# Kernel tuning notes

Hardware: AMD Instinct MI355X
Metric: run time of the kernel (lower is better)

Reference implementation:

```python
import jax, jax.numpy as jnp
import numpy as np

NV, NC = 100000, 50000        # num variables, num constraints
DV, DC = 8, 16                # padded neighbor-list widths
DIN, DH = 32, 128             # init_input_dim, output_dim (=init_output_dim)
NUM_LAYERS = 3                # aggregate loop runs num_layers-1 times
DCAT = 2 * DH + DIN           # input_dim of fc_variable/fc_constraint


def setup_inputs() -> dict:
    key = jax.random.key(0)
    ks = jax.random.split(key, 10)
    w = lambda k, shape: (jax.random.normal(k, shape, jnp.float32) * 0.05)
    return {
        "x": jax.random.normal(ks[0], (NV + NC, DIN), jnp.float32),
        "var_constr_index": jax.random.randint(ks[1], (NV, DV), 0, NC, dtype=jnp.int32),
        "constr_var_index": jax.random.randint(ks[2], (NC, DC), 0, NV, dtype=jnp.int32),
        "W_init_v": w(ks[3], (DIN, DH)), "b_init_v": jnp.zeros((DH,), jnp.float32),
        "W_init_c": w(ks[4], (DIN, DH)), "b_init_c": jnp.zeros((DH,), jnp.float32),
        "W_var": w(ks[5], (DCAT, DH)), "b_var": jnp.zeros((DH,), jnp.float32),
        "W_con": w(ks[6], (DCAT, DH)), "b_con": jnp.zeros((DH,), jnp.float32),
        "W_q": w(ks[7], (2 * DH, 1)), "b_q": jnp.zeros((1,), jnp.float32),
    }


def reference(x, var_constr_index, constr_var_index,
              W_init_v, b_init_v, W_init_c, b_init_c,
              W_var, b_var, W_con, b_con, W_q, b_q):
    nv = var_constr_index.shape[0]
    xv, xc = x[:nv], x[nv:]
    # layer zero init (fc_init_variables / fc_init_constraints)
    v = xv @ W_init_v + b_init_v          # [NV, DH]
    c = xc @ W_init_c + b_init_c          # [NC, DH]
    # message-passing layers: both updates read OLD v and OLD c
    for _ in range(1, NUM_LAYERS):
        agg_c = jnp.sum(v[constr_var_index], axis=1)   # [NC, DH] gather+sum over variable neighbors
        agg_v = jnp.sum(c[var_constr_index], axis=1)   # [NV, DH] gather+sum over constraint neighbors
        c_new = jnp.concatenate([agg_c, c, xc], axis=1) @ W_con + b_con
        v_new = jnp.concatenate([agg_v, v, xv], axis=1) @ W_var + b_var
        c, v = c_new, v_new
    # embedding_Q: global sum of variable features, broadcast, concat, linear
    g = jnp.sum(v, axis=0)                             # [DH]
    q_in = jnp.concatenate([jnp.broadcast_to(g, v.shape), v], axis=1)  # [NV, 2*DH]
    return q_in @ W_q + b_q                            # [NV, 1]
```

## Files before the change

kernel.cpp:

```cpp
#include <hip/hip_runtime.h>

#define NV 100000
#define NC 50000
#define DVAR 8
#define DCON 16

using short8 = __attribute__((ext_vector_type(8))) short;
using f32x4  = __attribute__((ext_vector_type(4))) float;

typedef const __attribute__((address_space(1))) void* as1cv;
typedef __attribute__((address_space(3))) void* as3v;

__device__ __forceinline__ unsigned short f2bf(float f) {
    union { float f; unsigned int u; } v; v.f = f;
    return (unsigned short)((v.u + 0x7fffu + ((v.u >> 16) & 1u)) >> 16);
}
__device__ __forceinline__ float bflo(unsigned int u) {
    union { unsigned int u; float f; } v; v.u = u << 16; return v.f;
}
__device__ __forceinline__ float bfhi(unsigned int u) {
    union { unsigned int u; float f; } v; v.u = u & 0xffff0000u; return v.f;
}

__global__ __launch_bounds__(256) void pack_kernel(
    const float* __restrict__ Wvar, const float* __restrict__ Wcon,
    const float* __restrict__ Wiv,  const float* __restrict__ Wic,
    unsigned short* __restrict__ WbVar, unsigned short* __restrict__ WbCon,
    unsigned short* __restrict__ WbIv,  unsigned short* __restrict__ WbIc,
    float* __restrict__ S)
{
    const int tid = blockIdx.x * 256 + threadIdx.x;
    for (int i = tid; i < 9 * 128 * 32; i += gridDim.x * 256) {
        int s = i >> 12, rem = i & 4095, c = rem >> 5, k = rem & 31;
        int src = (s * 32 + k) * 128 + c;
        WbVar[i] = f2bf(Wvar[src]);
        WbCon[i] = f2bf(Wcon[src]);
    }
    for (int i = tid; i < 128 * 32; i += gridDim.x * 256) {
        int c = i >> 5, k = i & 31;
        int src = k * 128 + c;
        WbIv[i] = f2bf(Wiv[src]);
        WbIc[i] = f2bf(Wic[src]);
    }
    if (tid == 0) S[0] = 0.f;
}

__global__ __launch_bounds__(256) void init_mfma(
    const float* __restrict__ x,
    const unsigned short* __restrict__ Wb,
    const float* __restrict__ bias,
    unsigned short* __restrict__ hout, int M)
{
    const int t = threadIdx.x;
    const int lane = t & 63;
    const int w = t >> 6;
    const int lrow = lane & 15;
    const int lg = lane >> 4;
    const int wrow0 = blockIdx.x * 64 + w * 16;
    int arow = wrow0 + lrow;
    int arowc = arow < M ? arow : M - 1;

    const float4* xp = (const float4*)(x + (size_t)arowc * 32 + lg * 8);
    float4 xa = xp[0], xb = xp[1];
    short8 afr;
    afr[0] = (short)f2bf(xa.x); afr[1] = (short)f2bf(xa.y);
    afr[2] = (short)f2bf(xa.z); afr[3] = (short)f2bf(xa.w);
    afr[4] = (short)f2bf(xb.x); afr[5] = (short)f2bf(xb.y);
    afr[6] = (short)f2bf(xb.z); afr[7] = (short)f2bf(xb.w);

    #pragma unroll
    for (int ct = 0; ct < 8; ++ct) {
        int c = ct * 16 + lrow;
        short8 bfr = *(const short8*)(Wb + (size_t)c * 32 + lg * 8);
        f32x4 acc = {0.f, 0.f, 0.f, 0.f};
        acc = __builtin_amdgcn_mfma_f32_16x16x32_bf16(afr, bfr, acc, 0, 0, 0);
        float bv = bias[c];
        #pragma unroll
        for (int r = 0; r < 4; ++r) {
            int orow = wrow0 + lg * 4 + r;
            if (orow < M) hout[(size_t)orow * 128 + c] = f2bf(acc[r] + bv);
        }
    }
}

template<int DEG>
__global__ __launch_bounds__(256) void agg_bf16(
    const unsigned short* __restrict__ hnb, const int* __restrict__ idx,
    unsigned short* __restrict__ agg, int M)
{
    const int tid = blockIdx.x * 256 + threadIdx.x;
    const int row = tid >> 4;
    const int part = tid & 15;
    if (row >= M) return;
    int nb[DEG];
    #pragma unroll
    for (int d4 = 0; d4 < DEG / 4; ++d4)
        *(int4*)(&nb[d4 * 4]) = *(const int4*)(idx + (size_t)row * DEG + d4 * 4);
    float a0=0.f,a1=0.f,a2=0.f,a3=0.f,a4=0.f,a5=0.f,a6=0.f,a7=0.f;
    #pragma unroll
    for (int b = 0; b < DEG; b += 8) {
        uint4 q[8];
        #pragma unroll
        for (int j = 0; j < 8; ++j)
            q[j] = *(const uint4*)(hnb + (size_t)nb[b + j] * 128 + part * 8);
        #pragma unroll
        for (int j = 0; j < 8; ++j) {
            a0 += bflo(q[j].x); a1 += bfhi(q[j].x);
            a2 += bflo(q[j].y); a3 += bfhi(q[j].y);
            a4 += bflo(q[j].z); a5 += bfhi(q[j].z);
            a6 += bflo(q[j].w); a7 += bfhi(q[j].w);
        }
    }
    uint4 o;
    o.x = (unsigned)f2bf(a0) | ((unsigned)f2bf(a1) << 16);
    o.y = (unsigned)f2bf(a2) | ((unsigned)f2bf(a3) << 16);
    o.z = (unsigned)f2bf(a4) | ((unsigned)f2bf(a5) << 16);
    o.w = (unsigned)f2bf(a6) | ((unsigned)f2bf(a7) << 16);
    *(uint4*)(agg + (size_t)row * 128 + part * 8) = o;
}

template<bool FINAL>
__global__ __launch_bounds__(256, 2) void gemm_mfma(
    const unsigned short* hself,
    const unsigned short* __restrict__ aggin,
    const float* __restrict__ xself,
    const unsigned short* __restrict__ Wb,
    const float* __restrict__ bias,
    unsigned short* hout,
    const float* __restrict__ Wq, float* __restrict__ S, float* __restrict__ dotout,
    int M)
{
    __shared__ __align__(16) unsigned short Aagg[64 * 128];
    __shared__ __align__(16) unsigned short Aself[64 * 128];
    __shared__ float red[4];
    const int t = threadIdx.x;
    const int lane = t & 63;
    const int w = t >> 6;
    const int lrow = lane & 15;
    const int lg = lane >> 4;
    const int r0 = blockIdx.x * 64;
    const int wrow0 = r0 + w * 16;
    const int arow = wrow0 + lrow;
    const int arowc = arow < M ? arow : M - 1;

    short8 xfr;
    {
        const float4* xp = (const float4*)(xself + (size_t)arowc * 32 + lg * 8);
        float4 xa = xp[0], xb = xp[1];
        xfr[0] = (short)f2bf(xa.x); xfr[1] = (short)f2bf(xa.y);
        xfr[2] = (short)f2bf(xa.z); xfr[3] = (short)f2bf(xa.w);
        xfr[4] = (short)f2bf(xb.x); xfr[5] = (short)f2bf(xb.y);
        xfr[6] = (short)f2bf(xb.z); xfr[7] = (short)f2bf(xb.w);
    }

    #pragma unroll
    for (int i = 0; i < 4; ++i) {
        int L = i * 256 + t;
        int row = L >> 4, c = L & 15;
        int gr = r0 + row;
        int grc = gr < M ? gr : M - 1;
        int cs = c ^ (row & 7);
        __builtin_amdgcn_global_load_lds(
            (as1cv)(aggin + (size_t)grc * 128 + cs * 8),
            (as3v)(&Aagg[(size_t)L * 8]), 16, 0, 0);
        __builtin_amdgcn_global_load_lds(
            (as1cv)(hself + (size_t)grc * 128 + cs * 8),
            (as3v)(&Aself[(size_t)L * 8]), 16, 0, 0);
    }

    short8 bfr[2][8];
    #pragma unroll
    for (int ct = 0; ct < 8; ++ct)
        bfr[0][ct] = *(const short8*)(Wb + (size_t)(ct * 16 + lrow) * 32 + lg * 8);

    __syncthreads();

    auto ldsA = [&](const unsigned short* base, int srel) -> short8 {
        int chunk = (4 * srel + lg) ^ (lrow & 7);
        return *(const short8*)(base + ((size_t)(w * 16 + lrow) * 16 + chunk) * 8);
    };

    f32x4 acc[8];
    #pragma unroll
    for (int ct = 0; ct < 8; ++ct) acc[ct] = (f32x4){0.f, 0.f, 0.f, 0.f};

    short8 afr = ldsA(Aagg, 0);
    #pragma unroll
    for (int s = 0; s < 9; ++s) {
        const int cur = s & 1, nxt = cur ^ 1;
        short8 afr_nxt;
        if (s < 8) {
            #pragma unroll
            for (int ct = 0; ct < 8; ++ct)
                bfr[nxt][ct] = *(const short8*)(
                    Wb + ((size_t)(s + 1) * 128 + ct * 16 + lrow) * 32 + lg * 8);
            afr_nxt = (s + 1 < 4) ? ldsA(Aagg, s + 1)
                    : (s + 1 < 8) ? ldsA(Aself, s + 1 - 4)
                                  : xfr;
        }
        #pragma unroll
        for (int ct = 0; ct < 8; ++ct)
            acc[ct] = __builtin_amdgcn_mfma_f32_16x16x32_bf16(afr, bfr[cur][ct], acc[ct], 0, 0, 0);
        afr = afr_nxt;
    }

    if (!FINAL) {
        #pragma unroll
        for (int ct = 0; ct < 8; ++ct) {
            int c = ct * 16 + lrow;
            float bv = bias[c];
            #pragma unroll
            for (int r = 0; r < 4; ++r) {
                int orow = wrow0 + lg * 4 + r;
                if (orow < M) hout[(size_t)orow * 128 + c] = f2bf(acc[ct][r] + bv);
            }
        }
    } else {
        float d0[4] = {0.f, 0.f, 0.f, 0.f};
        float d1[4] = {0.f, 0.f, 0.f, 0.f};
        #pragma unroll
        for (int ct = 0; ct < 8; ++ct) {
            int c = ct * 16 + lrow;
            float bv = bias[c];
            float wq0 = Wq[c];
            float wq1 = Wq[128 + c];
            #pragma unroll
            for (int r = 0; r < 4; ++r) {
                int orow = wrow0 + lg * 4 + r;
                float val = (orow < M) ? (acc[ct][r] + bv) : 0.f;
                d0[r] += val * wq0;
                d1[r] += val * wq1;
            }
        }
        #pragma unroll
        for (int r = 0; r < 4; ++r) {
            d0[r] += __shfl_xor(d0[r], 1); d0[r] += __shfl_xor(d0[r], 2);
            d0[r] += __shfl_xor(d0[r], 4); d0[r] += __shfl_xor(d0[r], 8);
            d1[r] += __shfl_xor(d1[r], 1); d1[r] += __shfl_xor(d1[r], 2);
            d1[r] += __shfl_xor(d1[r], 4); d1[r] += __shfl_xor(d1[r], 8);
        }
        if (lrow == 0) {
            #pragma unroll
            for (int r = 0; r < 4; ++r) {
                int orow = wrow0 + lg * 4 + r;
                if (orow < M) dotout[orow] = d1[r];
            }
        }
        float tot = d0[0] + d0[1] + d0[2] + d0[3];
        tot += __shfl_xor(tot, 16);
        tot += __shfl_xor(tot, 32);
        if (lane == 0) red[w] = tot;
        __syncthreads();
        if (t == 0) atomicAdd(S, red[0] + red[1] + red[2] + red[3]);
    }
}

__global__ __launch_bounds__(256) void addout_kernel(
    float* __restrict__ outp, const float* __restrict__ S,
    const float* __restrict__ bq, int n)
{
    int i = blockIdx.x * 256 + threadIdx.x;
    if (i < n) outp[i] = outp[i] + S[0] + bq[0];
}

extern "C" void kernel_launch(void* const* d_in, const int* in_sizes, int n_in,
                              void* d_out, int out_size, void* d_ws, size_t ws_size,
                              hipStream_t stream)
{
    const float* x    = (const float*)d_in[0];
    const int*   vci  = (const int*)  d_in[1];
    const int*   cvi  = (const int*)  d_in[2];
    const float* Wiv  = (const float*)d_in[3];
    const float* biv  = (const float*)d_in[4];
    const float* Wic  = (const float*)d_in[5];
    const float* bic  = (const float*)d_in[6];
    const float* Wvar = (const float*)d_in[7];
    const float* bvar = (const float*)d_in[8];
    const float* Wcon = (const float*)d_in[9];
    const float* bcon = (const float*)d_in[10];
    const float* Wq   = (const float*)d_in[11];
    const float* bq   = (const float*)d_in[12];
    float* outp = (float*)d_out;

    unsigned short* us = (unsigned short*)d_ws;
    size_t o = 0;
    unsigned short* vA    = us + o; o += (size_t)NV * 128;
    unsigned short* cA    = us + o; o += (size_t)NC * 128;
    unsigned short* cB    = us + o; o += (size_t)NC * 128;
    unsigned short* aggV  = us + o; o += (size_t)NV * 128;
    unsigned short* aggC  = us + o; o += (size_t)NC * 128;
    unsigned short* WbVar = us + o; o += 9 * 128 * 32;
    unsigned short* WbCon = us + o; o += 9 * 128 * 32;
    unsigned short* WbIv  = us + o; o += 128 * 32;
    unsigned short* WbIc  = us + o; o += 128 * 32;
    float* S = (float*)(us + o);

    const float* xc = x + (size_t)NV * 32;

    pack_kernel<<<144, 256, 0, stream>>>(Wvar, Wcon, Wiv, Wic, WbVar, WbCon, WbIv, WbIc, S);
    init_mfma<<<(NV + 63) / 64, 256, 0, stream>>>(x,  WbIv, biv, vA, NV);
    init_mfma<<<(NC + 63) / 64, 256, 0, stream>>>(xc, WbIc, bic, cA, NC);

    agg_bf16<DCON><<<(NC * 16 + 255) / 256, 256, 0, stream>>>(vA, cvi, aggC, NC);
    agg_bf16<DVAR><<<(NV * 16 + 255) / 256, 256, 0, stream>>>(cA, vci, aggV, NV);
    gemm_mfma<false><<<(NC + 63) / 64, 256, 0, stream>>>(
        cA, aggC, xc, WbCon, bcon, cB, nullptr, nullptr, nullptr, NC);
    gemm_mfma<false><<<(NV + 63) / 64, 256, 0, stream>>>(
        vA, aggV, x, WbVar, bvar, vA, nullptr, nullptr, nullptr, NV);

    agg_bf16<DVAR><<<(NV * 16 + 255) / 256, 256, 0, stream>>>(cB, vci, aggV, NV);
    gemm_mfma<true><<<(NV + 63) / 64, 256, 0, stream>>>(
        vA, aggV, x, WbVar, bvar, nullptr, Wq, S, outp, NV);

    addout_kernel<<<(NV + 255) / 256, 256, 0, stream>>>(outp, S, bq, NV);
}
```

Baseline: 298.3 us.

## Make GEMM persistent with double-buffered LDS tiles and pre-packed bf16 x

The fused GEMM kernel becomes persistent on a fixed 512-block grid. Each block loops over row tiles and stages the next tile's aggregate, self features and x into a second LDS buffer while computing the current one. A new kernel converts x to bf16 once up front, so the GEMMs load it straight into LDS and no longer convert floats per block. The aim is to hide global-load latency behind MFMA work and remove the repeated conversion, at the cost of an extra launch and roughly twice the LDS per block, which may limit occupancy.

```diff
diff --git a/kernel.cpp b/kernel.cpp
--- a/kernel.cpp
+++ b/kernel.cpp
@@ -43,6 +43,21 @@
         WbIc[i] = f2bf(Wic[src]);
     }
     if (tid == 0) S[0] = 0.f;
+}
+
+__global__ __launch_bounds__(256) void xpack_kernel(
+    const float* __restrict__ x, unsigned short* __restrict__ xb, int n8)
+{
+    int i = blockIdx.x * 256 + threadIdx.x;
+    if (i >= n8) return;
+    const float4* p = (const float4*)(x + (size_t)i * 8);
+    float4 a = p[0], b = p[1];
+    uint4 o;
+    o.x = (unsigned)f2bf(a.x) | ((unsigned)f2bf(a.y) << 16);
+    o.y = (unsigned)f2bf(a.z) | ((unsigned)f2bf(a.w) << 16);
+    o.z = (unsigned)f2bf(b.x) | ((unsigned)f2bf(b.y) << 16);
+    o.w = (unsigned)f2bf(b.z) | ((unsigned)f2bf(b.w) << 16);
+    *(uint4*)(xb + (size_t)i * 8) = o;
 }
 
 __global__ __launch_bounds__(256) void init_mfma(
@@ -123,133 +138,159 @@
 __global__ __launch_bounds__(256, 2) void gemm_mfma(
     const unsigned short* hself,
     const unsigned short* __restrict__ aggin,
-    const float* __restrict__ xself,
+    const unsigned short* __restrict__ xbself,
     const unsigned short* __restrict__ Wb,
     const float* __restrict__ bias,
     unsigned short* hout,
     const float* __restrict__ Wq, float* __restrict__ S, float* __restrict__ dotout,
     int M)
 {
-    __shared__ __align__(16) unsigned short Aagg[64 * 128];
-    __shared__ __align__(16) unsigned short Aself[64 * 128];
+    __shared__ __align__(16) unsigned short A0a[64 * 128], A0s[64 * 128];
+    __shared__ __align__(16) unsigned short A1a[64 * 128], A1s[64 * 128];
+    __shared__ __align__(16) unsigned short X0[64 * 32],  X1[64 * 32];
     __shared__ float red[4];
     const int t = threadIdx.x;
     const int lane = t & 63;
     const int w = t >> 6;
     const int lrow = lane & 15;
     const int lg = lane >> 4;
-    const int r0 = blockIdx.x * 64;
-    const int wrow0 = r0 + w * 16;
-    const int arow = wrow0 + lrow;
-    const int arowc = arow < M ? arow : M - 1;
-
-    short8 xfr;
-    {
-        const float4* xp = (const float4*)(xself + (size_t)arowc * 32 + lg * 8);
-        float4 xa = xp[0], xb = xp[1];
-        xfr[0] = (short)f2bf(xa.x); xfr[1] = (short)f2bf(xa.y);
-        xfr[2] = (short)f2bf(xa.z); xfr[3] = (short)f2bf(xa.w);
-        xfr[4] = (short)f2bf(xb.x); xfr[5] = (short)f2bf(xb.y);
-        xfr[6] = (short)f2bf(xb.z); xfr[7] = (short)f2bf(xb.w);
-    }
-
-    #pragma unroll
-    for (int i = 0; i < 4; ++i) {
-        int L = i * 256 + t;
-        int row = L >> 4, c = L & 15;
-        int gr = r0 + row;
-        int grc = gr < M ? gr : M - 1;
-        int cs = c ^ (row & 7);
-        __builtin_amdgcn_global_load_lds(
-            (as1cv)(aggin + (size_t)grc * 128 + cs * 8),
-            (as3v)(&Aagg[(size_t)L * 8]), 16, 0, 0);
-        __builtin_amdgcn_global_load_lds(
-            (as1cv)(hself + (size_t)grc * 128 + cs * 8),
-            (as3v)(&Aself[(size_t)L * 8]), 16, 0, 0);
-    }
-
-    short8 bfr[2][8];
-    #pragma unroll
-    for (int ct = 0; ct < 8; ++ct)
-        bfr[0][ct] = *(const short8*)(Wb + (size_t)(ct * 16 + lrow) * 32 + lg * 8);
-
-    __syncthreads();
-
-    auto ldsA = [&](const unsigned short* base, int srel) -> short8 {
-        int chunk = (4 * srel + lg) ^ (lrow & 7);
-        return *(const short8*)(base + ((size_t)(w * 16 + lrow) * 16 + chunk) * 8);
+    const int ntiles = (M + 63) >> 6;
+
+    float Sacc = 0.f;
+
+    auto stage = [&](unsigned short* La, unsigned short* Ls, unsigned short* Lx, int tile) {
+        const int r0 = tile * 64;
+        #pragma unroll
+        for (int i = 0; i < 4; ++i) {
+            int L = i * 256 + t;
+            int row = L >> 4, c = L & 15;
+            int gr = r0 + row;
+            int grc = gr < M ? gr : M - 1;
+            int cs = c ^ (row & 7);
+            __builtin_amdgcn_global_load_lds((as1cv)(aggin + (size_t)grc * 128 + cs * 8),
+                                             (as3v)(La + (size_t)L * 8), 16, 0, 0);
+            __builtin_amdgcn_global_load_lds((as1cv)(hself + (size_t)grc * 128 + cs * 8),
+                                             (as3v)(Ls + (size_t)L * 8), 16, 0, 0);
+        }
+        {
+            int row = t >> 2, c = t & 3;
+            int gr = r0 + row;
+            int grc = gr < M ? gr : M - 1;
+            int cs = c ^ (row & 3);
+            __builtin_amdgcn_global_load_lds((as1cv)(xbself + (size_t)grc * 32 + cs * 8),
+                                             (as3v)(Lx + (size_t)t * 8), 16, 0, 0);
+        }
     };
 
-    f32x4 acc[8];
-    #pragma unroll
-    for (int ct = 0; ct < 8; ++ct) acc[ct] = (f32x4){0.f, 0.f, 0.f, 0.f};
-
-    short8 afr = ldsA(Aagg, 0);
-    #pragma unroll
-    for (int s = 0; s < 9; ++s) {
-        const int cur = s & 1, nxt = cur ^ 1;
-        short8 afr_nxt;
-        if (s < 8) {
+    auto compute = [&](const unsigned short* La, const unsigned short* Ls,
+                       const unsigned short* Lx, int tile) {
+        const int wrow0 = tile * 64 + w * 16;
+        auto dsA = [&](const unsigned short* base, int srel) -> short8 {
+            int chunk = (4 * srel + lg) ^ (lrow & 7);
+            return *(const short8*)(base + ((size_t)(w * 16 + lrow) * 16 + chunk) * 8);
+        };
+        short8 bA[8], bB[8];
+        #pragma unroll
+        for (int ct = 0; ct < 8; ++ct)
+            bA[ct] = *(const short8*)(Wb + (size_t)(ct * 16 + lrow) * 32 + lg * 8);
+        short8 afr = dsA(La, 0);
+        f32x4 acc[8];
+        #pragma unroll
+        for (int ct = 0; ct < 8; ++ct) acc[ct] = (f32x4){0.f, 0.f, 0.f, 0.f};
+
+        #pragma unroll
+        for (int s = 0; s < 9; ++s) {
+            short8 anext;
+            if (s < 8) {
+                short8* bn = (s & 1) ? bA : bB;
+                #pragma unroll
+                for (int ct = 0; ct < 8; ++ct)
+                    bn[ct] = *(const short8*)(
+                        Wb + ((size_t)(s + 1) * 128 + ct * 16 + lrow) * 32 + lg * 8);
+                if (s + 1 < 4)      anext = dsA(La, s + 1);
+                else if (s + 1 < 8) anext = dsA(Ls, s + 1 - 4);
+                else {
+                    int chunk = lg ^ (lrow & 3);
+                    anext = *(const short8*)(Lx + ((size_t)(w * 16 + lrow) * 4 + chunk) * 8);
+                }
+            }
+            const short8* bc = (s & 1) ? bB : bA;
             #pragma unroll
             for (int ct = 0; ct < 8; ++ct)
-                bfr[nxt][ct] = *(const short8*)(
-                    Wb + ((size_t)(s + 1) * 128 + ct * 16 + lrow) * 32 + lg * 8);
-            afr_nxt = (s + 1 < 4) ? ldsA(Aagg, s + 1)
-                    : (s + 1 < 8) ? ldsA(Aself, s + 1 - 4)
-                                  : xfr;
-        }
-        #pragma unroll
-        for (int ct = 0; ct < 8; ++ct)
-            acc[ct] = __builtin_amdgcn_mfma_f32_16x16x32_bf16(afr, bfr[cur][ct], acc[ct], 0, 0, 0);
-        afr = afr_nxt;
-    }
-
-    if (!FINAL) {
-        #pragma unroll
-        for (int ct = 0; ct < 8; ++ct) {
-            int c = ct * 16 + lrow;
-            float bv = bias[c];
+                acc[ct] = __builtin_amdgcn_mfma_f32_16x16x32_bf16(afr, bc[ct], acc[ct], 0, 0, 0);
+            afr = anext;
+        }
+
+        if (!FINAL) {
+            #pragma unroll
+            for (int ct = 0; ct < 8; ++ct) {
+                int c = ct * 16 + lrow;
+                float bv = bias[c];
+                #pragma unroll
+                for (int r = 0; r < 4; ++r) {
+                    int orow = wrow0 + lg * 4 + r;
+                    if (orow < M) hout[(size_t)orow * 128 + c] = f2bf(acc[ct][r] + bv);
+                }
+            }
+        } else {
+            float d0[4] = {0.f, 0.f, 0.f, 0.f};
+            float d1[4] = {0.f, 0.f, 0.f, 0.f};
+            #pragma unroll
+            for (int ct = 0; ct < 8; ++ct) {
+                int c = ct * 16 + lrow;
+                float bv = bias[c];
+                float wq0 = Wq[c];
+                float wq1 = Wq[128 + c];
+                #pragma unroll
+                for (int r = 0; r < 4; ++r) {
+                    int orow = wrow0 + lg * 4 + r;
+                    float val = (orow < M) ? (acc[ct][r] + bv) : 0.f;
+                    d0[r] += val * wq0;
+                    d1[r] += val * wq1;
+                }
+            }
             #pragma unroll
             for (int r = 0; r < 4; ++r) {
-                int orow = wrow0 + lg * 4 + r;
-                if (orow < M) hout[(size_t)orow * 128 + c] = f2bf(acc[ct][r] + bv);
-            }
-        }
-    } else {
-        float d0[4] = {0.f, 0.f, 0.f, 0.f};
-        float d1[4] = {0.f, 0.f, 0.f, 0.f};
-        #pragma unroll
-        for (int ct = 0; ct < 8; ++ct) {
-            int c = ct * 16 + lrow;
-            float bv = bias[c];
-            float wq0 = Wq[c];
-            float wq1 = Wq[128 + c];
-            #pragma unroll
-            for (int r = 0; r < 4; ++r) {
-                int orow = wrow0 + lg * 4 + r;
-                float val = (orow < M) ? (acc[ct][r] + bv) : 0.f;
-                d0[r] += val * wq0;
-                d1[r] += val * wq1;
-            }
-        }
-        #pragma unroll
-        for (int r = 0; r < 4; ++r) {
-            d0[r] += __shfl_xor(d0[r], 1); d0[r] += __shfl_xor(d0[r], 2);
-            d0[r] += __shfl_xor(d0[r], 4); d0[r] += __shfl_xor(d0[r], 8);
-            d1[r] += __shfl_xor(d1[r], 1); d1[r] += __shfl_xor(d1[r], 2);
-            d1[r] += __shfl_xor(d1[r], 4); d1[r] += __shfl_xor(d1[r], 8);
-        }
-        if (lrow == 0) {
-            #pragma unroll
-            for (int r = 0; r < 4; ++r) {
-                int orow = wrow0 + lg * 4 + r;
-                if (orow < M) dotout[orow] = d1[r];
-            }
-        }
-        float tot = d0[0] + d0[1] + d0[2] + d0[3];
-        tot += __shfl_xor(tot, 16);
-        tot += __shfl_xor(tot, 32);
-        if (lane == 0) red[w] = tot;
+                d0[r] += __shfl_xor(d0[r], 1); d0[r] += __shfl_xor(d0[r], 2);
+                d0[r] += __shfl_xor(d0[r], 4); d0[r] += __shfl_xor(d0[r], 8);
+                d1[r] += __shfl_xor(d1[r], 1); d1[r] += __shfl_xor(d1[r], 2);
+                d1[r] += __shfl_xor(d1[r], 4); d1[r] += __shfl_xor(d1[r], 8);
+            }
+            if (lrow == 0) {
+                #pragma unroll
+                for (int r = 0; r < 4; ++r) {
+                    int orow = wrow0 + lg * 4 + r;
+                    if (orow < M) dotout[orow] = d1[r];
+                }
+            }
+            float tot = d0[0] + d0[1] + d0[2] + d0[3];
+            tot += __shfl_xor(tot, 16);
+            tot += __shfl_xor(tot, 32);
+            Sacc += tot;
+        }
+    };
+
+    int tile = blockIdx.x;
+    if (tile < ntiles) {
+        stage(A0a, A0s, X0, tile);
+        __syncthreads();
+        while (true) {
+            int nxt = tile + gridDim.x;
+            if (nxt < ntiles) stage(A1a, A1s, X1, nxt);
+            compute(A0a, A0s, X0, tile);
+            __syncthreads();
+            if (nxt >= ntiles) break;
+            tile = nxt;
+            nxt = tile + gridDim.x;
+            if (nxt < ntiles) stage(A0a, A0s, X0, nxt);
+            compute(A1a, A1s, X1, tile);
+            __syncthreads();
+            if (nxt >= ntiles) break;
+            tile = nxt;
+        }
+    }
+    if (FINAL) {
+        if (lane == 0) red[w] = Sacc;
         __syncthreads();
         if (t == 0) atomicAdd(S, red[0] + red[1] + red[2] + red[3]);
     }
@@ -289,6 +330,8 @@
     unsigned short* cB    = us + o; o += (size_t)NC * 128;
     unsigned short* aggV  = us + o; o += (size_t)NV * 128;
     unsigned short* aggC  = us + o; o += (size_t)NC * 128;
+    unsigned short* xbV   = us + o; o += (size_t)NV * 32;
+    unsigned short* xbC   = us + o; o += (size_t)NC * 32;
     unsigned short* WbVar = us + o; o += 9 * 128 * 32;
     unsigned short* WbCon = us + o; o += 9 * 128 * 32;
     unsigned short* WbIv  = us + o; o += 128 * 32;
@@ -298,19 +341,20 @@
     const float* xc = x + (size_t)NV * 32;
 
     pack_kernel<<<144, 256, 0, stream>>>(Wvar, Wcon, Wiv, Wic, WbVar, WbCon, WbIv, WbIc, S);
+    xpack_kernel<<<((NV + NC) * 4 + 255) / 256, 256, 0, stream>>>(x, xbV, (NV + NC) * 4);
     init_mfma<<<(NV + 63) / 64, 256, 0, stream>>>(x,  WbIv, biv, vA, NV);
     init_mfma<<<(NC + 63) / 64, 256, 0, stream>>>(xc, WbIc, bic, cA, NC);
 
     agg_bf16<DCON><<<(NC * 16 + 255) / 256, 256, 0, stream>>>(vA, cvi, aggC, NC);
     agg_bf16<DVAR><<<(NV * 16 + 255) / 256, 256, 0, stream>>>(cA, vci, aggV, NV);
-    gemm_mfma<false><<<(NC + 63) / 64, 256, 0, stream>>>(
-        cA, aggC, xc, WbCon, bcon, cB, nullptr, nullptr, nullptr, NC);
-    gemm_mfma<false><<<(NV + 63) / 64, 256, 0, stream>>>(
-        vA, aggV, x, WbVar, bvar, vA, nullptr, nullptr, nullptr, NV);
+    gemm_mfma<false><<<512, 256, 0, stream>>>(
+        cA, aggC, xbC, WbCon, bcon, cB, nullptr, nullptr, nullptr, NC);
+    gemm_mfma<false><<<512, 256, 0, stream>>>(
+        vA, aggV, xbV, WbVar, bvar, vA, nullptr, nullptr, nullptr, NV);
 
     agg_bf16<DVAR><<<(NV * 16 + 255) / 256, 256, 0, stream>>>(cB, vci, aggV, NV);
-    gemm_mfma<true><<<(NV + 63) / 64, 256, 0, stream>>>(
-        vA, aggV, x, WbVar, bvar, nullptr, Wq, S, outp, NV);
+    gemm_mfma<true><<<512, 256, 0, stream>>>(
+        vA, aggV, xbV, WbVar, bvar, nullptr, Wq, S, outp, NV);
 
     addout_kernel<<<(NV + 255) / 256, 256, 0, stream>>>(outp, S, bq, NV);
 }
```

After: 476.6 us. 59.8% more time.
